# Kernel optimization log

Measured on AMD Instinct MI355X. Metric: run time of the kernel, lower is better.

## Reference

```python
import jax, jax.numpy as jnp
import numpy as np
import math

B, N, D, O, H = 2, 3072, 64, 64, 4

def setup_inputs() -> dict:
    key = jax.random.key(0)
    ks = jax.random.split(key, 8)
    x = jax.random.normal(ks[0], (B, N, D), dtype=jnp.float32)
    edge_index = jax.random.randint(ks[1], (B, N, N), 0, 2, dtype=jnp.int32)
    s = 1.0 / math.sqrt(D)
    Wv = jax.random.uniform(ks[2], (H, D, O), jnp.float32, -s, s)
    bv = jax.random.uniform(ks[3], (H, O), jnp.float32, -s, s)
    Wq = jax.random.uniform(ks[4], (H, D, O), jnp.float32, -s, s)
    bq = jax.random.uniform(ks[5], (H, O), jnp.float32, -s, s)
    Wk = jax.random.uniform(ks[6], (H, D, O), jnp.float32, -s, s)
    bk = jax.random.uniform(ks[7], (H, O), jnp.float32, -s, s)
    return {"x": x, "edge_index": edge_index, "Wv": Wv, "bv": bv,
            "Wq": Wq, "bq": bq, "Wk": Wk, "bk": bk}

def reference(x, edge_index, Wv, bv, Wq, bq, Wk, bk):
    # x: [B,N,D]; edge_index: dense {0,1} adjacency [B,N,N]
    dk = jnp.asarray(math.sqrt(x.shape[-1]), x.dtype)
    v = jnp.einsum('bnd,hdo->bhno', x, Wv) + bv[None, :, None, :]
    q = jnp.einsum('bnd,hdo->bhno', x, Wq) + bq[None, :, None, :]
    k = jnp.einsum('bnd,hdo->bhno', x, Wk) + bk[None, :, None, :]
    scores = jnp.einsum('bhno,bhmo->bhnm', q, k) / dk        # [B,H,N,N]
    scores = jax.nn.leaky_relu(scores, 0.2)
    mask = (-1e10) * (1.0 - edge_index.astype(scores.dtype))  # [B,N,N]
    scores = scores + mask[:, None, :, :]
    prop = jax.nn.softmax(scores, axis=-1)
    # dropout on v omitted (inference mode: identity)
    feats = jnp.einsum('bhnm,bhmo->bhno', prop, v)            # [B,H,N,O]
    out = jnp.mean(feats, axis=1)                             # [B,N,O]
    return jax.nn.leaky_relu(out, 0.2)
```

## Files before the change

kernel.cpp:

```cpp
#include <hip/hip_runtime.h>
#include <hip/hip_bf16.h>
#include <cstdint>

#define Bc 2
#define Nc 3072
#define Hc 4
#define NW32 96
#define TILEB 8192
#define KSC 4
#define TPS (NW32/KSC)

typedef __bf16    bf16x8 __attribute__((ext_vector_type(8)));
typedef _Float16  f16x8  __attribute__((ext_vector_type(8)));
typedef float     f32x16 __attribute__((ext_vector_type(16)));

#define QSCALE 0.18033688f

static __device__ __forceinline__ f32x16 mfma32bf(bf16x8 a, bf16x8 b, f32x16 c) {
    return __builtin_amdgcn_mfma_f32_32x32x16_bf16(a, b, c, 0, 0, 0);
}
static __device__ __forceinline__ f32x16 mfma32h(f16x8 a, f16x8 b, f32x16 c) {
    return __builtin_amdgcn_mfma_f32_32x32x16_f16(a, b, c, 0, 0, 0);
}
static __device__ __forceinline__ uint32_t pkrtz(float lo, float hi) {
    uint32_t w;
    asm("v_cvt_pkrtz_f16_f32 %0, %1, %2" : "=v"(w) : "v"(lo), "v"(hi));
    return w;
}

static __device__ __forceinline__ void softmax_pack(const f32x16& sc, uint32_t mwh,
                                                    uint32_t W8[8], float& lsum)
{
    #pragma unroll
    for (int i = 0; i < 8; ++i) {
        const int bp0 = (2*i & 3) + 8*(2*i >> 2);
        float s0 = sc[2*i], s1 = sc[2*i + 1];
        float a0 = fmaxf(s0, 0.2f*s0);
        float a1 = fmaxf(s1, 0.2f*s1);
        float e0, e1;
        asm("v_exp_f32 %0, %1" : "=v"(e0) : "v"(a0));
        asm("v_exp_f32 %0, %1" : "=v"(e1) : "v"(a1));
        uint32_t m0 = (uint32_t)(((int)(mwh << (31 - bp0))) >> 31);
        uint32_t m1 = (uint32_t)(((int)(mwh << (30 - bp0))) >> 31);
        float p0 = __uint_as_float(__float_as_uint(e0) & m0);
        float p1 = __uint_as_float(__float_as_uint(e1) & m1);
        lsum += p0 + p1;
        W8[i] = pkrtz(p0, p1);
    }
}

static __device__ __forceinline__ void assemble_pa(uint32_t W8[8], f16x8& pa0, f16x8& pa1)
{
    uint32_t a0 = W8[0], a2 = W8[2], a1 = W8[1], a3 = W8[3];
    uint32_t b0 = W8[4], b2 = W8[6], b1 = W8[5], b3 = W8[7];
    asm("v_permlane32_swap_b32 %0, %1" : "+v"(a0), "+v"(a2));
    asm("v_permlane32_swap_b32 %0, %1" : "+v"(a1), "+v"(a3));
    asm("v_permlane32_swap_b32 %0, %1" : "+v"(b0), "+v"(b2));
    asm("v_permlane32_swap_b32 %0, %1" : "+v"(b1), "+v"(b3));
    union { uint32_t u[4]; f16x8 v; } u0, u1;
    u0.u[0] = a0; u0.u[1] = a1; u0.u[2] = a2; u0.u[3] = a3;
    u1.u[0] = b0; u1.u[1] = b1; u1.u[2] = b2; u1.u[3] = b3;
    pa0 = u0.v; pa1 = u1.v;
}

static __device__ __forceinline__ void load_subtile(const char* gt, int hi, int l31,
                                                    f16x8 (&K)[4], f16x8 (&V)[4])
{
    #pragma unroll
    for (int kk = 0; kk < 4; ++kk)
        K[kk] = *(const f16x8*)(gt + ((kk*2 + hi) << 9) + (l31 << 4));
    #pragma unroll
    for (int i = 0; i < 4; ++i) {
        const int kkp = i >> 1, ot = i & 1;
        V[i] = *(const f16x8*)(gt + 4096 + ((kkp*2 + hi) << 10) + ((ot*32 + l31) << 4));
    }
}

static __device__ __forceinline__ void compute_subtile(
    const f16x8 (&K)[4], const f16x8 (&V)[4], uint32_t mw, int hi,
    const f16x8 (&qf)[4], const f32x16& fzero,
    f32x16& acc0, f32x16& acc1, float& lsum)
{
    f32x16 sc;
    __builtin_amdgcn_s_setprio(1);
    sc = mfma32h(K[0], qf[0], fzero);
    sc = mfma32h(K[1], qf[1], sc);
    sc = mfma32h(K[2], qf[2], sc);
    sc = mfma32h(K[3], qf[3], sc);
    __builtin_amdgcn_s_setprio(0);

    uint32_t W8[8];
    softmax_pack(sc, mw >> (hi*4), W8, lsum);
    f16x8 pa0, pa1;
    assemble_pa(W8, pa0, pa1);

    __builtin_amdgcn_s_setprio(1);
    acc0 = mfma32h(pa0, V[0], acc0);
    acc1 = mfma32h(pa0, V[1], acc1);
    acc0 = mfma32h(pa1, V[2], acc0);
    acc1 = mfma32h(pa1, V[3], acc1);
    __builtin_amdgcn_s_setprio(0);
}

__global__ void prep_kernel(const float* __restrict__ Wq, const float* __restrict__ Wk,
                            const float* __restrict__ Wv,
                            const float* __restrict__ bq, const float* __restrict__ bk,
                            const float* __restrict__ bv,
                            __bf16* __restrict__ Wbh, __bf16* __restrict__ Wbl,
                            float* __restrict__ Bs)
{
    int i = blockIdx.x*256 + threadIdx.x;
    int d = i & 63, o = (i >> 6) & 63, h = (i >> 12) & 3, p = i >> 14;
    const float* W = (p == 0) ? Wq : (p == 1) ? Wk : Wv;
    float scale = (p == 0) ? QSCALE : 1.0f;
    float val = W[(h*64 + d)*64 + o] * scale;
    int idx = (((p*Hc + h)*64 + o) << 6) + d;
    __bf16 hi = (__bf16)val;
    Wbh[idx] = hi;
    Wbl[idx] = (__bf16)(val - (float)hi);
    if (i < 3*Hc*64) {
        int pp = i / (Hc*64), rest = i % (Hc*64);
        const float* B = (pp == 0) ? bq : (pp == 1) ? bk : bv;
        Bs[i] = B[rest] * ((pp == 0) ? QSCALE : 1.0f);
    }
}

__global__ __launch_bounds__(256) void qkv_mfma(
    const float* __restrict__ x,
    const __bf16* __restrict__ Wbh, const __bf16* __restrict__ Wbl,
    const float* __restrict__ Bs,
    _Float16* __restrict__ Qf, _Float16* __restrict__ Kf,
    _Float16* __restrict__ KVimg)
{
    const int lane = threadIdx.x & 63, w = threadIdx.x >> 6;
    const int l31 = lane & 31, hi = lane >> 5;
    int t = blockIdx.x;
    int nt = t % 48; t /= 48;
    int b  = t & 1;  t >>= 1;
    int p  = t % 3;
    int h  = t / 3;
    const int r0 = (w >> 1)*32, c0 = (w & 1)*32, n0 = nt*64;

    bf16x8 xh[4], xl[4], wh[4], wl[4];
    #pragma unroll
    for (int kk = 0; kk < 4; ++kk) {
        size_t xoff = (((size_t)(b*Nc + n0 + r0 + l31)) << 6) + kk*16 + hi*8;
        float4 f0 = *(const float4*)(x + xoff);
        float4 f1 = *(const float4*)(x + xoff + 4);
        float xs[8] = {f0.x, f0.y, f0.z, f0.w, f1.x, f1.y, f1.z, f1.w};
        #pragma unroll
        for (int j = 0; j < 8; ++j) {
            __bf16 hh = (__bf16)xs[j];
            xh[kk][j] = hh;
            xl[kk][j] = (__bf16)(xs[j] - (float)hh);
        }
        size_t woff = (((size_t)((p*Hc + h)*64 + c0 + l31)) << 6) + kk*16 + hi*8;
        wh[kk] = *(const bf16x8*)(Wbh + woff);
        wl[kk] = *(const bf16x8*)(Wbl + woff);
    }
    float bias = Bs[(p*Hc + h)*64 + c0 + l31];
    f32x16 acc;
    #pragma unroll
    for (int i = 0; i < 16; ++i) acc[i] = bias;
    #pragma unroll
    for (int kk = 0; kk < 4; ++kk) {
        acc = mfma32bf(xh[kk], wh[kk], acc);
        acc = mfma32bf(xl[kk], wh[kk], acc);
        acc = mfma32bf(xh[kk], wl[kk], acc);
    }
    const int bh = b*Hc + h;
    if (p < 2) {
        _Float16* dst = (p == 0) ? Qf : Kf;
        #pragma unroll
        for (int r = 0; r < 16; ++r) {
            int row = (r & 3) + 8*(r >> 2) + 4*hi;
            size_t idx = (((size_t)bh*Nc + n0 + r0 + row) << 6) + c0 + l31;
            dst[idx] = (_Float16)acc[r];
        }
    } else {
        const int t_img = (n0 + r0) >> 5;
        char* img = (char*)KVimg + (size_t)(bh*96 + t_img)*TILEB;
        #pragma unroll
        for (int grp = 0; grp < 2; ++grp) {
            uint32_t wH[4];
            #pragma unroll
            for (int j = 0; j < 4; ++j)
                wH[j] = pkrtz(acc[grp*8 + 2*j], acc[grp*8 + 2*j + 1]);
            asm("v_permlane32_swap_b32 %0, %1" : "+v"(wH[0]), "+v"(wH[2]));
            asm("v_permlane32_swap_b32 %0, %1" : "+v"(wH[1]), "+v"(wH[3]));
            const int kb = grp*2 + hi;
            const int o  = c0 + l31;
            uint4 gh = {wH[0], wH[1], wH[2], wH[3]};
            *(uint4*)(img + 4096 + ((kb*64 + o) << 4)) = gh;
        }
    }
}

__global__ void imgk_kernel(const _Float16* __restrict__ Kf, _Float16* __restrict__ KVimg)
{
    const int t = blockIdx.x % 96, bh = blockIdx.x / 96;
    char* img = (char*)KVimg + (size_t)(bh*96 + t)*TILEB;
    int dc = threadIdx.x & 7, key = threadIdx.x >> 3;
    size_t src = (((size_t)bh*Nc + t*32 + key) << 6) + dc*8;
    *(uint4*)(img + (dc*32 + key)*16) = *(const uint4*)(Kf + src);
}

__global__ void pack_kernel(const int* __restrict__ edge, uint32_t* __restrict__ pmT)
{
    int gw = blockIdx.x*4 + (threadIdx.x >> 6);
    int lane = threadIdx.x & 63;
    int ng = gw % 48; gw /= 48;
    int w  = gw % NW32; gw /= NW32;
    int b  = gw;
    int n = ng*64 + lane;
    const uint4* ep = (const uint4*)(edge + ((size_t)b*Nc + n)*Nc + w*32);
    uint32_t word = 0;
    #pragma unroll
    for (int i = 0; i < 8; ++i) {
        uint4 e = ep[i];
        word |= (e.x ? 1u : 0u) << (4*i);
        word |= (e.y ? 1u : 0u) << (4*i + 1);
        word |= (e.z ? 1u : 0u) << (4*i + 2);
        word |= (e.w ? 1u : 0u) << (4*i + 3);
    }
    pmT[((size_t)b*NW32 + w)*Nc + n] = word;
}

__global__ __launch_bounds__(256, 3) void attn_mfma(
    const _Float16* __restrict__ Qf,
    const _Float16* __restrict__ KVimg, const uint32_t* __restrict__ pmT,
    float* __restrict__ PA, float* __restrict__ PL)
{
    const int lane = threadIdx.x & 63, w = threadIdx.x >> 6;
    const int l31 = lane & 31, hi = lane >> 5;
    int gb = blockIdx.x;
    const int bh = gb & 7; gb >>= 3;
    const int qt = gb % 24;
    const int ks = gb / 24;
    const int b = bh >> 2;
    const int qrow0 = qt*128 + w*32;
    const int t0 = ks*TPS;

    const uint32_t* pmp = pmT + ((size_t)b*NW32 + t0)*Nc + qrow0 + l31;
    const char* gt = (const char*)KVimg + (size_t)(bh*96 + t0)*TILEB;

    f16x8 qf[4];
    #pragma unroll
    for (int kk = 0; kk < 4; ++kk) {
        size_t qoff = (((size_t)bh*Nc + qrow0 + l31) << 6) + kk*16 + hi*8;
        qf[kk] = *(const f16x8*)(Qf + qoff);
    }
    f32x16 fzero;
    #pragma unroll
    for (int i = 0; i < 16; ++i) fzero[i] = 0.f;

    f32x16 acc0 = fzero, acc1 = fzero;
    float lsum = 0.f;

    f16x8 KA[4], VA[4], KB[4], VB[4];
    uint32_t mwA, mwB;
    load_subtile(gt, hi, l31, KA, VA);
    mwA = pmp[0];

    #pragma unroll 1
    for (int j = 0; j < TPS/2; ++j) {
        load_subtile(gt + (size_t)(2*j + 1)*TILEB, hi, l31, KB, VB);
        mwB = pmp[(size_t)(2*j + 1)*Nc];
        compute_subtile(KA, VA, mwA, hi, qf, fzero, acc0, acc1, lsum);
        const int tn = (2*j + 2 < TPS) ? (2*j + 2) : 0;
        load_subtile(gt + (size_t)tn*TILEB, hi, l31, KA, VA);
        mwA = pmp[(size_t)tn*Nc];
        compute_subtile(KB, VB, mwB, hi, qf, fzero, acc0, acc1, lsum);
    }

    lsum += __shfl_xor(lsum, 32);
    float* po = PA + (((size_t)(bh*KSC + ks)*Nc + qrow0) << 6);
    #pragma unroll
    for (int r = 0; r < 16; ++r) {
        int row = (r & 3) + 8*(r >> 2) + 4*hi;
        po[((size_t)row << 6) + l31]      = acc0[r];
        po[((size_t)row << 6) + 32 + l31] = acc1[r];
    }
    if (lane < 32)
        PL[(size_t)(bh*KSC + ks)*Nc + qrow0 + l31] = lsum;
}

__global__ void merge_kernel(const float* __restrict__ PA, const float* __restrict__ PL,
                             float* __restrict__ out)
{
    int gid = blockIdx.x*256 + threadIdx.x;
    int o  = gid & 63;
    int bn = gid >> 6;
    int n  = bn % Nc;
    int b  = bn / Nc;
    float ft = 0.f;
    for (int h = 0; h < Hc; ++h) {
        int bh = b*Hc + h;
        float A = 0.f, L = 0.f;
        for (int ks = 0; ks < KSC; ++ks) {
            A += PA[(((size_t)(bh*KSC + ks)*Nc + n) << 6) + o];
            L += PL[(size_t)(bh*KSC + ks)*Nc + n];
        }
        ft += A / L;
    }
    ft *= 0.25f;
    out[((size_t)bn << 6) + o] = fmaxf(ft, 0.f) + 0.2f*fminf(ft, 0.f);
}

extern "C" void kernel_launch(void* const* d_in, const int* in_sizes, int n_in,
                              void* d_out, int out_size, void* d_ws, size_t ws_size,
                              hipStream_t stream)
{
    const float* x    = (const float*)d_in[0];
    const int*   edge = (const int*)d_in[1];
    const float* Wv   = (const float*)d_in[2];
    const float* bv   = (const float*)d_in[3];
    const float* Wq   = (const float*)d_in[4];
    const float* bq   = (const float*)d_in[5];
    const float* Wk   = (const float*)d_in[6];
    const float* bk   = (const float*)d_in[7];
    float* out = (float*)d_out;

    const size_t PROJ = (size_t)Bc*Hc*Nc*64;
    char* p = (char*)d_ws;
    __bf16* Wbh = (__bf16*)p;     p += 49152*2;
    __bf16* Wbl = (__bf16*)p;     p += 49152*2;
    float*  Bs  = (float*)p;      p += 4096;
    _Float16* Qf = (_Float16*)p;  p += PROJ*2;
    _Float16* Kf = (_Float16*)p;  p += PROJ*2;
    _Float16* KVimg = (_Float16*)p; p += (size_t)Bc*Hc*96*TILEB;
    uint32_t* pmT = (uint32_t*)p; p += (size_t)Bc*NW32*Nc*4;
    float* PA = (float*)p;        p += (size_t)Bc*Hc*KSC*Nc*64*4;
    float* PL = (float*)p;

    hipLaunchKernelGGL(prep_kernel, dim3(192),  dim3(256), 0, stream,
                       Wq, Wk, Wv, bq, bk, bv, Wbh, Wbl, Bs);
    hipLaunchKernelGGL(qkv_mfma,    dim3(1152), dim3(256), 0, stream,
                       x, Wbh, Wbl, Bs, Qf, Kf, KVimg);
    hipLaunchKernelGGL(imgk_kernel, dim3(Bc*Hc*96), dim3(256), 0, stream, Kf, KVimg);
    hipLaunchKernelGGL(pack_kernel, dim3(Bc*NW32*48/4), dim3(256), 0, stream, edge, pmT);
    hipLaunchKernelGGL(attn_mfma,   dim3(8*KSC*24), dim3(256), 0, stream,
                       Qf, KVimg, pmT, PA, PL);
    hipLaunchKernelGGL(merge_kernel, dim3((Bc*Nc*64)/256), dim3(256), 0, stream,
                       PA, PL, out);
}
```

Before: 78.65 us.

## Fuse prep and pack kernels, drop K image, split keys further, dot2 row sums

Merges the weight-prep and adjacency bit-pack kernels into one launch and removes the separate K image kernel, so the attention kernel reads K directly from the row-major Kf buffer and V from its own image. KSC doubles from 4 to 8 and the occupancy hint goes from 3 to 4 waves, giving more blocks for the attention stage at the cost of a larger partial buffer and more merge work. The softmax masks the packed fp16 pair and accumulates the row sum with a v_dot2 instruction instead of separate float adds. Row sums now come from fp16-rounded values, which may shift accuracy slightly.

```diff
diff --git a/kernel.cpp b/kernel.cpp
--- a/kernel.cpp
+++ b/kernel.cpp
@@ -6,8 +6,7 @@
 #define Nc 3072
 #define Hc 4
 #define NW32 96
-#define TILEB 8192
-#define KSC 4
+#define KSC 8
 #define TPS (NW32/KSC)
 
 typedef __bf16    bf16x8 __attribute__((ext_vector_type(8)));
@@ -29,7 +28,8 @@
 }
 
 static __device__ __forceinline__ void softmax_pack(const f32x16& sc, uint32_t mwh,
-                                                    uint32_t W8[8], float& lsum)
+                                                    uint32_t W8[8], float& lsum,
+                                                    uint32_t ones32)
 {
     #pragma unroll
     for (int i = 0; i < 8; ++i) {
@@ -40,12 +40,12 @@
         float e0, e1;
         asm("v_exp_f32 %0, %1" : "=v"(e0) : "v"(a0));
         asm("v_exp_f32 %0, %1" : "=v"(e1) : "v"(a1));
+        uint32_t pk = pkrtz(e0, e1);
         uint32_t m0 = (uint32_t)(((int)(mwh << (31 - bp0))) >> 31);
         uint32_t m1 = (uint32_t)(((int)(mwh << (30 - bp0))) >> 31);
-        float p0 = __uint_as_float(__float_as_uint(e0) & m0);
-        float p1 = __uint_as_float(__float_as_uint(e1) & m1);
-        lsum += p0 + p1;
-        W8[i] = pkrtz(p0, p1);
+        uint32_t wv = pk & ((m0 & 0x0000ffffu) | (m1 & 0xffff0000u));
+        W8[i] = wv;
+        asm("v_dot2_f32_f16 %0, %1, %2, %0" : "+v"(lsum) : "v"(wv), "v"(ones32));
     }
 }
 
@@ -63,22 +63,23 @@
     pa0 = u0.v; pa1 = u1.v;
 }
 
-static __device__ __forceinline__ void load_subtile(const char* gt, int hi, int l31,
+static __device__ __forceinline__ void load_subtile(const char* gk, const char* gv,
+                                                    int hi, int l31,
                                                     f16x8 (&K)[4], f16x8 (&V)[4])
 {
     #pragma unroll
     for (int kk = 0; kk < 4; ++kk)
-        K[kk] = *(const f16x8*)(gt + ((kk*2 + hi) << 9) + (l31 << 4));
+        K[kk] = *(const f16x8*)(gk + ((kk*2 + hi) << 4));
     #pragma unroll
     for (int i = 0; i < 4; ++i) {
         const int kkp = i >> 1, ot = i & 1;
-        V[i] = *(const f16x8*)(gt + 4096 + ((kkp*2 + hi) << 10) + ((ot*32 + l31) << 4));
+        V[i] = *(const f16x8*)(gv + ((kkp*2 + hi) << 10) + ((ot*32 + l31) << 4));
     }
 }
 
 static __device__ __forceinline__ void compute_subtile(
     const f16x8 (&K)[4], const f16x8 (&V)[4], uint32_t mw, int hi,
-    const f16x8 (&qf)[4], const f32x16& fzero,
+    const f16x8 (&qf)[4], const f32x16& fzero, uint32_t ones32,
     f32x16& acc0, f32x16& acc1, float& lsum)
 {
     f32x16 sc;
@@ -90,7 +91,7 @@
     __builtin_amdgcn_s_setprio(0);
 
     uint32_t W8[8];
-    softmax_pack(sc, mw >> (hi*4), W8, lsum);
+    softmax_pack(sc, mw >> (hi*4), W8, lsum, ones32);
     f16x8 pa0, pa1;
     assemble_pa(W8, pa0, pa1);
 
@@ -102,26 +103,47 @@
     __builtin_amdgcn_s_setprio(0);
 }
 
-__global__ void prep_kernel(const float* __restrict__ Wq, const float* __restrict__ Wk,
-                            const float* __restrict__ Wv,
-                            const float* __restrict__ bq, const float* __restrict__ bk,
-                            const float* __restrict__ bv,
-                            __bf16* __restrict__ Wbh, __bf16* __restrict__ Wbl,
-                            float* __restrict__ Bs)
-{
-    int i = blockIdx.x*256 + threadIdx.x;
-    int d = i & 63, o = (i >> 6) & 63, h = (i >> 12) & 3, p = i >> 14;
-    const float* W = (p == 0) ? Wq : (p == 1) ? Wk : Wv;
-    float scale = (p == 0) ? QSCALE : 1.0f;
-    float val = W[(h*64 + d)*64 + o] * scale;
-    int idx = (((p*Hc + h)*64 + o) << 6) + d;
-    __bf16 hi = (__bf16)val;
-    Wbh[idx] = hi;
-    Wbl[idx] = (__bf16)(val - (float)hi);
-    if (i < 3*Hc*64) {
-        int pp = i / (Hc*64), rest = i % (Hc*64);
-        const float* B = (pp == 0) ? bq : (pp == 1) ? bk : bv;
-        Bs[i] = B[rest] * ((pp == 0) ? QSCALE : 1.0f);
+__global__ void preppack_kernel(const float* __restrict__ Wq, const float* __restrict__ Wk,
+                                const float* __restrict__ Wv,
+                                const float* __restrict__ bq, const float* __restrict__ bk,
+                                const float* __restrict__ bv,
+                                const int* __restrict__ edge,
+                                __bf16* __restrict__ Wbh, __bf16* __restrict__ Wbl,
+                                float* __restrict__ Bs, uint32_t* __restrict__ pmT)
+{
+    if (blockIdx.x < 192) {
+        int i = blockIdx.x*256 + threadIdx.x;
+        int d = i & 63, o = (i >> 6) & 63, h = (i >> 12) & 3, p = i >> 14;
+        const float* W = (p == 0) ? Wq : (p == 1) ? Wk : Wv;
+        float scale = (p == 0) ? QSCALE : 1.0f;
+        float val = W[(h*64 + d)*64 + o] * scale;
+        int idx = (((p*Hc + h)*64 + o) << 6) + d;
+        __bf16 hi = (__bf16)val;
+        Wbh[idx] = hi;
+        Wbl[idx] = (__bf16)(val - (float)hi);
+        if (i < 3*Hc*64) {
+            int pp = i / (Hc*64), rest = i % (Hc*64);
+            const float* B = (pp == 0) ? bq : (pp == 1) ? bk : bv;
+            Bs[i] = B[rest] * ((pp == 0) ? QSCALE : 1.0f);
+        }
+    } else {
+        int gw = (blockIdx.x - 192)*4 + (threadIdx.x >> 6);
+        int lane = threadIdx.x & 63;
+        int ng = gw % 48; gw /= 48;
+        int w  = gw % NW32; gw /= NW32;
+        int b  = gw;
+        int n = ng*64 + lane;
+        const uint4* ep = (const uint4*)(edge + ((size_t)b*Nc + n)*Nc + w*32);
+        uint32_t word = 0;
+        #pragma unroll
+        for (int i = 0; i < 8; ++i) {
+            uint4 e = ep[i];
+            word |= (e.x ? 1u : 0u) << (4*i);
+            word |= (e.y ? 1u : 0u) << (4*i + 1);
+            word |= (e.z ? 1u : 0u) << (4*i + 2);
+            word |= (e.w ? 1u : 0u) << (4*i + 3);
+        }
+        pmT[((size_t)b*NW32 + w)*Nc + n] = word;
     }
 }
 
@@ -130,7 +152,7 @@
     const __bf16* __restrict__ Wbh, const __bf16* __restrict__ Wbl,
     const float* __restrict__ Bs,
     _Float16* __restrict__ Qf, _Float16* __restrict__ Kf,
-    _Float16* __restrict__ KVimg)
+    _Float16* __restrict__ Vimg)
 {
     const int lane = threadIdx.x & 63, w = threadIdx.x >> 6;
     const int l31 = lane & 31, hi = lane >> 5;
@@ -179,7 +201,7 @@
         }
     } else {
         const int t_img = (n0 + r0) >> 5;
-        char* img = (char*)KVimg + (size_t)(bh*96 + t_img)*TILEB;
+        char* img = (char*)Vimg + (((size_t)(bh*96 + t_img)) << 12);
         #pragma unroll
         for (int grp = 0; grp < 2; ++grp) {
             uint32_t wH[4];
@@ -191,44 +213,14 @@
             const int kb = grp*2 + hi;
             const int o  = c0 + l31;
             uint4 gh = {wH[0], wH[1], wH[2], wH[3]};
-            *(uint4*)(img + 4096 + ((kb*64 + o) << 4)) = gh;
-        }
-    }
-}
-
-__global__ void imgk_kernel(const _Float16* __restrict__ Kf, _Float16* __restrict__ KVimg)
-{
-    const int t = blockIdx.x % 96, bh = blockIdx.x / 96;
-    char* img = (char*)KVimg + (size_t)(bh*96 + t)*TILEB;
-    int dc = threadIdx.x & 7, key = threadIdx.x >> 3;
-    size_t src = (((size_t)bh*Nc + t*32 + key) << 6) + dc*8;
-    *(uint4*)(img + (dc*32 + key)*16) = *(const uint4*)(Kf + src);
-}
-
-__global__ void pack_kernel(const int* __restrict__ edge, uint32_t* __restrict__ pmT)
-{
-    int gw = blockIdx.x*4 + (threadIdx.x >> 6);
-    int lane = threadIdx.x & 63;
-    int ng = gw % 48; gw /= 48;
-    int w  = gw % NW32; gw /= NW32;
-    int b  = gw;
-    int n = ng*64 + lane;
-    const uint4* ep = (const uint4*)(edge + ((size_t)b*Nc + n)*Nc + w*32);
-    uint32_t word = 0;
-    #pragma unroll
-    for (int i = 0; i < 8; ++i) {
-        uint4 e = ep[i];
-        word |= (e.x ? 1u : 0u) << (4*i);
-        word |= (e.y ? 1u : 0u) << (4*i + 1);
-        word |= (e.z ? 1u : 0u) << (4*i + 2);
-        word |= (e.w ? 1u : 0u) << (4*i + 3);
-    }
-    pmT[((size_t)b*NW32 + w)*Nc + n] = word;
-}
-
-__global__ __launch_bounds__(256, 3) void attn_mfma(
-    const _Float16* __restrict__ Qf,
-    const _Float16* __restrict__ KVimg, const uint32_t* __restrict__ pmT,
+            *(uint4*)(img + ((kb*64 + o) << 4)) = gh;
+        }
+    }
+}
+
+__global__ __launch_bounds__(256, 4) void attn_mfma(
+    const _Float16* __restrict__ Qf, const _Float16* __restrict__ Kf,
+    const _Float16* __restrict__ Vimg, const uint32_t* __restrict__ pmT,
     float* __restrict__ PA, float* __restrict__ PL)
 {
     const int lane = threadIdx.x & 63, w = threadIdx.x >> 6;
@@ -242,7 +234,8 @@
     const int t0 = ks*TPS;
 
     const uint32_t* pmp = pmT + ((size_t)b*NW32 + t0)*Nc + qrow0 + l31;
-    const char* gt = (const char*)KVimg + (size_t)(bh*96 + t0)*TILEB;
+    const char* gk = (const char*)Kf + (((size_t)(bh*Nc + t0*32 + l31)) << 7);
+    const char* gv = (const char*)Vimg + (((size_t)(bh*96 + t0)) << 12);
 
     f16x8 qf[4];
     #pragma unroll
@@ -253,24 +246,26 @@
     f32x16 fzero;
     #pragma unroll
     for (int i = 0; i < 16; ++i) fzero[i] = 0.f;
+    const uint32_t ones32 = 0x3C003C00u;
 
     f32x16 acc0 = fzero, acc1 = fzero;
     float lsum = 0.f;
 
     f16x8 KA[4], VA[4], KB[4], VB[4];
     uint32_t mwA, mwB;
-    load_subtile(gt, hi, l31, KA, VA);
+    load_subtile(gk, gv, hi, l31, KA, VA);
     mwA = pmp[0];
 
     #pragma unroll 1
     for (int j = 0; j < TPS/2; ++j) {
-        load_subtile(gt + (size_t)(2*j + 1)*TILEB, hi, l31, KB, VB);
+        load_subtile(gk + (size_t)(2*j + 1)*4096, gv + (size_t)(2*j + 1)*4096,
+                     hi, l31, KB, VB);
         mwB = pmp[(size_t)(2*j + 1)*Nc];
-        compute_subtile(KA, VA, mwA, hi, qf, fzero, acc0, acc1, lsum);
+        compute_subtile(KA, VA, mwA, hi, qf, fzero, ones32, acc0, acc1, lsum);
         const int tn = (2*j + 2 < TPS) ? (2*j + 2) : 0;
-        load_subtile(gt + (size_t)tn*TILEB, hi, l31, KA, VA);
+        load_subtile(gk + (size_t)tn*4096, gv + (size_t)tn*4096, hi, l31, KA, VA);
         mwA = pmp[(size_t)tn*Nc];
-        compute_subtile(KB, VB, mwB, hi, qf, fzero, acc0, acc1, lsum);
+        compute_subtile(KB, VB, mwB, hi, qf, fzero, ones32, acc0, acc1, lsum);
     }
 
     lsum += __shfl_xor(lsum, 32);
@@ -328,19 +323,17 @@
     float*  Bs  = (float*)p;      p += 4096;
     _Float16* Qf = (_Float16*)p;  p += PROJ*2;
     _Float16* Kf = (_Float16*)p;  p += PROJ*2;
-    _Float16* KVimg = (_Float16*)p; p += (size_t)Bc*Hc*96*TILEB;
+    _Float16* Vimg = (_Float16*)p; p += ((size_t)Bc*Hc*96) << 12;
     uint32_t* pmT = (uint32_t*)p; p += (size_t)Bc*NW32*Nc*4;
     float* PA = (float*)p;        p += (size_t)Bc*Hc*KSC*Nc*64*4;
     float* PL = (float*)p;
 
-    hipLaunchKernelGGL(prep_kernel, dim3(192),  dim3(256), 0, stream,
-                       Wq, Wk, Wv, bq, bk, bv, Wbh, Wbl, Bs);
+    hipLaunchKernelGGL(preppack_kernel, dim3(192 + Bc*NW32*48/4), dim3(256), 0, stream,
+                       Wq, Wk, Wv, bq, bk, bv, edge, Wbh, Wbl, Bs, pmT);
     hipLaunchKernelGGL(qkv_mfma,    dim3(1152), dim3(256), 0, stream,
-                       x, Wbh, Wbl, Bs, Qf, Kf, KVimg);
-    hipLaunchKernelGGL(imgk_kernel, dim3(Bc*Hc*96), dim3(256), 0, stream, Kf, KVimg);
-    hipLaunchKernelGGL(pack_kernel, dim3(Bc*NW32*48/4), dim3(256), 0, stream, edge, pmT);
+                       x, Wbh, Wbl, Bs, Qf, Kf, Vimg);
     hipLaunchKernelGGL(attn_mfma,   dim3(8*KSC*24), dim3(256), 0, stream,
-                       Qf, KVimg, pmT, PA, PL);
+                       Qf, Kf, Vimg, pmT, PA, PL);
     hipLaunchKernelGGL(merge_kernel, dim3((Bc*Nc*64)/256), dim3(256), 0, stream,
                        PA, PL, out);
 }
```

Measured after the change: 130.3 us. +65.6%, slower.
